# Optimization experiments

Hardware: AMD Instinct MI355X
Metric: run time of the kernel (lower is better)

The kernel has to match this reference:

```python
import jax, jax.numpy as jnp
import numpy as np

B, L, D = 16, 4096, 512
HORIZON = 100.0


def setup_inputs() -> dict:
    key = jax.random.key(0)
    k1, k2, k3 = jax.random.split(key, 3)
    tokens = jax.random.normal(k1, (B, L, D), dtype=jnp.float32)
    # ragged lengths in [1, L]
    lengths = jax.random.randint(k2, (B,), 1, L + 1, dtype=jnp.int32)
    cls = jax.random.normal(k3, (D,), dtype=jnp.float32)
    return {"tokens": tokens, "lengths": lengths, "cls": cls}


def reference(tokens, lengths, cls):
    # tokens: [B, L, D] padded ragged batch, lengths: [B], cls: [D]
    Bb, Ll, Dd = tokens.shape
    pos = jnp.arange(Ll, dtype=tokens.dtype)[:, None]            # [L, 1]
    idx = jnp.arange(Dd, dtype=tokens.dtype)[None, :]            # [1, D]
    freq = 1.0 / HORIZON ** ((idx - idx % 2) / Dd)               # [1, D]
    phase = (jnp.pi / 2) * (idx % 2)                             # [1, D]
    emb = jnp.sin(pos @ (freq + phase))                          # [L, D] outer product, as in source

    x = tokens + emb[None]                                       # broadcast add over batch
    valid = jnp.arange(Ll)[None, :] < lengths[:, None]           # [B, L]
    x = jnp.where(valid[..., None], x, jnp.zeros((), tokens.dtype))

    # output: [B, L+1, D]; row `lengths[b]` of each sequence holds the CLS token
    out = jnp.zeros((Bb, Ll + 1, Dd), tokens.dtype).at[:, :Ll, :].set(x)
    cls_onehot = (jnp.arange(Ll + 1)[None, :] == lengths[:, None]).astype(tokens.dtype)
    out = out + cls_onehot[..., None] * cls[None, None, :]
    return out
```

## Files before the change

### kernel.cpp

```cpp
#include <hip/hip_runtime.h>

constexpr int Bc = 16;
constexpr int Lc = 4096;
constexpr int Dc = 512;
constexpr int D4 = Dc / 4;
constexpr int ROWS = Bc * (Lc + 1);
constexpr int TOTAL4 = ROWS * D4;

__global__ __launch_bounds__(256) void pe_kernel(
    const float* __restrict__ tokens,
    const int*   __restrict__ lengths,
    const float* __restrict__ cls,
    float*       __restrict__ out)
{
    int t = blockIdx.x * 256 + threadIdx.x;
    if (t >= TOTAL4) return;

    int d4  = t & (D4 - 1);
    int row = t >> 7;
    int b   = row / (Lc + 1);
    int l   = row - b * (Lc + 1);
    int len = lengths[b];
    int d0  = d4 << 2;

    float4 r;
    if (l < len) {
        const float4 tok = *reinterpret_cast<const float4*>(
            tokens + ((size_t)(b * Lc + l) << 9) + d0);

        const float K      = 6.6438561897747395f / 512.0f;
        const float INV2PI = 0.15915493667125702f;

        float f0 = __builtin_exp2f(-(float)d0       * K) * INV2PI;
        float f2 = __builtin_exp2f(-(float)(d0 + 2) * K) * INV2PI;
        float c0 = f0;
        float c1 = f0 + 0.25f;
        float c2 = f2;
        float c3 = f2 + 0.25f;

        float lf = (float)l;
        float r0 = __builtin_amdgcn_fractf(lf * c0);
        float r1 = __builtin_amdgcn_fractf(lf * c1);
        float r2 = __builtin_amdgcn_fractf(lf * c2);
        float r3 = __builtin_amdgcn_fractf(lf * c3);

        r.x = tok.x + __builtin_amdgcn_sinf(r0);
        r.y = tok.y + __builtin_amdgcn_sinf(r1);
        r.z = tok.z + __builtin_amdgcn_sinf(r2);
        r.w = tok.w + __builtin_amdgcn_sinf(r3);
    } else if (l == len) {
        r = *reinterpret_cast<const float4*>(cls + d0);
    } else {
        r = make_float4(0.f, 0.f, 0.f, 0.f);
    }

    reinterpret_cast<float4*>(out)[t] = r;
}

extern "C" void kernel_launch(void* const* d_in, const int* in_sizes, int n_in,
                              void* d_out, int out_size, void* d_ws, size_t ws_size,
                              hipStream_t stream) {
    const float* tokens  = (const float*)d_in[0];
    const int*   lengths = (const int*)d_in[1];
    const float* cls     = (const float*)d_in[2];
    float*       out     = (float*)d_out;

    int blocks = (TOTAL4 + 255) / 256;
    pe_kernel<<<blocks, 256, 0, stream>>>(tokens, lengths, cls, out);
}
```

Before: 211.0 us.

## Process 16 floats per thread with nontemporal I/O and recurrent frequencies

Each thread now handles a 64-byte chunk of a row (four 16-byte vectors) instead of a single float4, cutting the grid size and the per-element index arithmetic four-fold. Token loads and output stores use nontemporal builtins to avoid polluting the cache on this streaming workload. Per-pair frequencies come from a multiplicative recurrence (repeated multiply by a constant ratio) rather than one exp2 per pair. In exchange, lanes within a wave now access memory with a 64-byte stride per instruction, and the recurrence adds a small accumulated rounding error to the phase.

New measurement: 336.5 us. +59.4%, slower.

```diff
diff --git a/kernel.cpp b/kernel.cpp
--- a/kernel.cpp
+++ b/kernel.cpp
@@ -3,9 +3,13 @@
 constexpr int Bc = 16;
 constexpr int Lc = 4096;
 constexpr int Dc = 512;
-constexpr int D4 = Dc / 4;
-constexpr int ROWS = Bc * (Lc + 1);
-constexpr int TOTAL4 = ROWS * D4;
+constexpr int ROWSPB = Lc + 1;
+constexpr int ROWS = Bc * ROWSPB;
+constexpr int CH_PER_ROW = Dc / 16;
+constexpr int NCHUNK = ROWS * CH_PER_ROW;
+static_assert(NCHUNK % 256 == 0, "grid divides evenly");
+
+typedef float vf4 __attribute__((ext_vector_type(4)));
 
 __global__ __launch_bounds__(256) void pe_kernel(
     const float* __restrict__ tokens,
@@ -13,48 +17,60 @@
     const float* __restrict__ cls,
     float*       __restrict__ out)
 {
-    int t = blockIdx.x * 256 + threadIdx.x;
-    if (t >= TOTAL4) return;
+    int chunk = blockIdx.x * 256 + threadIdx.x;
+    int c   = chunk & (CH_PER_ROW - 1);
+    int row = chunk >> 5;
+    int b   = row / ROWSPB;
+    int l   = row - b * ROWSPB;
+    int d0  = c << 4;
+    int len = lengths[b];
 
-    int d4  = t & (D4 - 1);
-    int row = t >> 7;
-    int b   = row / (Lc + 1);
-    int l   = row - b * (Lc + 1);
-    int len = lengths[b];
-    int d0  = d4 << 2;
+    vf4 r[4];
 
-    float4 r;
     if (l < len) {
-        const float4 tok = *reinterpret_cast<const float4*>(
+        const vf4* tp = reinterpret_cast<const vf4*>(
             tokens + ((size_t)(b * Lc + l) << 9) + d0);
+        vf4 tok[4];
+        #pragma unroll
+        for (int i = 0; i < 4; ++i)
+            tok[i] = __builtin_nontemporal_load(tp + i);
 
         const float K      = 6.6438561897747395f / 512.0f;
         const float INV2PI = 0.15915493667125702f;
-
-        float f0 = __builtin_exp2f(-(float)d0       * K) * INV2PI;
-        float f2 = __builtin_exp2f(-(float)(d0 + 2) * K) * INV2PI;
-        float c0 = f0;
-        float c1 = f0 + 0.25f;
-        float c2 = f2;
-        float c3 = f2 + 0.25f;
+        const float R2     = 0.98217170f;
 
         float lf = (float)l;
-        float r0 = __builtin_amdgcn_fractf(lf * c0);
-        float r1 = __builtin_amdgcn_fractf(lf * c1);
-        float r2 = __builtin_amdgcn_fractf(lf * c2);
-        float r3 = __builtin_amdgcn_fractf(lf * c3);
+        float fe = __builtin_exp2f(-(float)d0 * K) * INV2PI;
 
-        r.x = tok.x + __builtin_amdgcn_sinf(r0);
-        r.y = tok.y + __builtin_amdgcn_sinf(r1);
-        r.z = tok.z + __builtin_amdgcn_sinf(r2);
-        r.w = tok.w + __builtin_amdgcn_sinf(r3);
+        #pragma unroll
+        for (int i = 0; i < 4; ++i) {
+            float s[4];
+            #pragma unroll
+            for (int j = 0; j < 2; ++j) {
+                float a0 = __builtin_amdgcn_fractf(lf * fe);
+                float a1 = __builtin_amdgcn_fractf(lf * (fe + 0.25f));
+                s[2*j]   = __builtin_amdgcn_sinf(a0);
+                s[2*j+1] = __builtin_amdgcn_sinf(a1);
+                fe *= R2;
+            }
+            r[i].x = tok[i].x + s[0];
+            r[i].y = tok[i].y + s[1];
+            r[i].z = tok[i].z + s[2];
+            r[i].w = tok[i].w + s[3];
+        }
     } else if (l == len) {
-        r = *reinterpret_cast<const float4*>(cls + d0);
+        const vf4* cp = reinterpret_cast<const vf4*>(cls + d0);
+        #pragma unroll
+        for (int i = 0; i < 4; ++i) r[i] = cp[i];
     } else {
-        r = make_float4(0.f, 0.f, 0.f, 0.f);
+        #pragma unroll
+        for (int i = 0; i < 4; ++i) r[i] = (vf4){0.f, 0.f, 0.f, 0.f};
     }
 
-    reinterpret_cast<float4*>(out)[t] = r;
+    vf4* op = reinterpret_cast<vf4*>(out + ((size_t)row << 9) + d0);
+    #pragma unroll
+    for (int i = 0; i < 4; ++i)
+        __builtin_nontemporal_store(r[i], op + i);
 }
 
 extern "C" void kernel_launch(void* const* d_in, const int* in_sizes, int n_in,
@@ -65,6 +81,5 @@
     const float* cls     = (const float*)d_in[2];
     float*       out     = (float*)d_out;
 
-    int blocks = (TOTAL4 + 255) / 256;
-    pe_kernel<<<blocks, 256, 0, stream>>>(tokens, lengths, cls, out);
+    pe_kernel<<<NCHUNK / 256, 256, 0, stream>>>(tokens, lengths, cls, out);
 }
```
